# Performance work log

Measured on AMD Instinct MI355X. Metric: run time of the kernel, lower is better.

The kernel has to match this reference:

```python
import jax, jax.numpy as jnp
import numpy as np

NEG_SLOPE = 0.01  # torch F.leaky_relu default

def leaky_relu(x):
    return jnp.where(x >= 0, x, NEG_SLOPE * x)

def setup_inputs() -> dict:
    key = jax.random.key(0)
    ks = jax.random.split(key, 16)
    N, D, H, L = 2048, 512, 256, 16
    # normalized-adjacency-like matrix: row sums ~0.5 to keep activations sane
    A_hat = jax.random.uniform(ks[0], (N, N), dtype=jnp.float32) / N
    X = jax.random.normal(ks[1], (N, D), dtype=jnp.float32)
    eps = jax.random.normal(ks[2], (N, L), dtype=jnp.float32)
    def lin(k, fan_out, fan_in):
        s = 1.0 / np.sqrt(fan_in)
        kw, kb = jax.random.split(k)
        W = jax.random.uniform(kw, (fan_out, fan_in), minval=-s, maxval=s, dtype=jnp.float32)
        b = jax.random.uniform(kb, (fan_out,), minval=-s, maxval=s, dtype=jnp.float32)
        return W, b
    W1, b1 = lin(ks[3], H, D)          # gcn1
    Wmu, bmu = lin(ks[4], L, H)        # gcn2_mu
    Wlv, blv = lin(ks[5], L, H)        # gcn2_logvar
    Wd1, bd1 = lin(ks[6], 2 * L, 2 * L)  # decoder_fc1
    Wd2, bd2 = lin(ks[7], 1, 2 * L)      # decoder_fc2
    return {"A_hat": A_hat, "X": X, "eps": eps,
            "W1": W1, "b1": b1, "Wmu": Wmu, "bmu": bmu,
            "Wlv": Wlv, "blv": blv, "Wd1": Wd1, "bd1": bd1,
            "Wd2": Wd2, "bd2": bd2}

def reference(A_hat, X, eps, W1, b1, Wmu, bmu, Wlv, blv, Wd1, bd1, Wd2, bd2):
    L = Wmu.shape[0]
    # --- encode: two GCN layers (A_hat @ X) @ W.T + b ---
    Hh = leaky_relu((A_hat @ X) @ W1.T + b1)           # [N, H]
    AH = A_hat @ Hh                                    # [N, H]
    mu = AH @ Wmu.T + bmu                              # [N, L]
    logvar = AH @ Wlv.T + blv                          # [N, L]
    # --- reparameterize ---
    Z = mu + eps * jnp.exp(0.5 * logvar)               # [N, L]
    # --- decode: pairwise MLP on concat(Z_i, Z_j), vectorized ---
    # fc1(concat(Zi,Zj)) = Zi @ Wd1[:, :L].T + Zj @ Wd1[:, L:].T + bd1
    P = Z @ Wd1[:, :L].T                               # [N, 2L]
    Q = Z @ Wd1[:, L:].T                               # [N, 2L]
    h = leaky_relu(P[:, None, :] + Q[None, :, :] + bd1)  # [N, N, 2L]
    A_pred = jax.nn.sigmoid(jnp.einsum('nmh,h->nm', h, Wd2[0]) + bd2[0])  # [N, N]
    return (A_pred, mu, logvar)
```

## Files before the change

### kernel.cpp

```cpp
#include <hip/hip_runtime.h>

#define NNODE 2048
#define DD    512
#define HHID  256
#define LLAT  16
#define H2    32

typedef __attribute__((ext_vector_type(8))) short  short8;
typedef __attribute__((ext_vector_type(4))) float  f32x4;

__device__ __forceinline__ unsigned short f2bf(float x) {
    unsigned int u = __float_as_uint(x);
    unsigned int r = (u + 0x7fffu + ((u >> 16) & 1u)) >> 16;
    return (unsigned short)r;
}
__device__ __forceinline__ float bf2f(unsigned short u) {
    return __uint_as_float(((unsigned int)u) << 16);
}

__global__ __launch_bounds__(256) void t0_cvt(const float* __restrict__ A,
                                              const float* __restrict__ X,
                                              const float* __restrict__ W1,
                                              unsigned short* __restrict__ Abf,
                                              unsigned short* __restrict__ Xbf,
                                              unsigned short* __restrict__ W1bf) {
    const int NT = 1343488;
    for (int v = blockIdx.x * 256 + threadIdx.x; v < NT; v += gridDim.x * 256) {
        const float* src; unsigned short* dst; int off;
        if (v < 1048576)      { src = A;  dst = Abf;  off = v; }
        else if (v < 1310720) { src = X;  dst = Xbf;  off = v - 1048576; }
        else                  { src = W1; dst = W1bf; off = v - 1310720; }
        float4 f = ((const float4*)src)[off];
        short4 h;
        h.x = (short)f2bf(f.x); h.y = (short)f2bf(f.y);
        h.z = (short)f2bf(f.z); h.w = (short)f2bf(f.w);
        ((short4*)dst)[off] = h;
    }
}

__global__ __launch_bounds__(256) void t1_mfma(const unsigned short* __restrict__ W1bf,
                                               const unsigned short* __restrict__ Xbf,
                                               unsigned short* __restrict__ XWt) {
    const int wt   = blockIdx.x * 4 + (threadIdx.x >> 6);
    const int lane = threadIdx.x & 63;
    const int h0 = (wt >> 7) * 16;
    const int n0 = (wt & 127) * 16;
    const int lm = lane & 15, lk = (lane >> 4) * 8;
    const unsigned short* ap = W1bf + (size_t)(h0 + lm) * DD + lk;
    const unsigned short* bp = Xbf  + (size_t)(n0 + lm) * DD + lk;
    f32x4 acc = {};
    #pragma unroll 4
    for (int k = 0; k < DD; k += 32) {
        short8 a = *(const short8*)(ap + k);
        short8 b = *(const short8*)(bp + k);
        acc = __builtin_amdgcn_mfma_f32_16x16x32_bf16(a, b, acc, 0, 0, 0);
    }
    const int col = n0 + lm;
    #pragma unroll
    for (int r = 0; r < 4; ++r) {
        int row = h0 + (lane >> 4) * 4 + r;
        XWt[(size_t)row * NNODE + col] = f2bf(acc[r]);
    }
}

__global__ __launch_bounds__(256) void t2_mfma(const unsigned short* __restrict__ Abf,
                                               const unsigned short* __restrict__ XWt,
                                               const float* __restrict__ bias1,
                                               unsigned short* __restrict__ Hbf) {
    const int wt   = blockIdx.x * 4 + (threadIdx.x >> 6);
    const int lane = threadIdx.x & 63;
    const int m0 = (wt >> 3) * 16;
    const int n0 = (wt & 7) * 32;
    const int lm = lane & 15, lk = (lane >> 4) * 8;
    const unsigned short* ap  = Abf + (size_t)(m0 + lm) * NNODE + lk;
    const unsigned short* bp0 = XWt + (size_t)(n0 + lm) * NNODE + lk;
    const unsigned short* bp1 = XWt + (size_t)(n0 + 16 + lm) * NNODE + lk;
    f32x4 acc0 = {}, acc1 = {};
    #pragma unroll 4
    for (int k = 0; k < NNODE; k += 32) {
        short8 a  = *(const short8*)(ap + k);
        short8 b0 = *(const short8*)(bp0 + k);
        short8 b1 = *(const short8*)(bp1 + k);
        acc0 = __builtin_amdgcn_mfma_f32_16x16x32_bf16(a, b0, acc0, 0, 0, 0);
        acc1 = __builtin_amdgcn_mfma_f32_16x16x32_bf16(a, b1, acc1, 0, 0, 0);
    }
    const int col0 = n0 + lm, col1 = n0 + 16 + lm;
    const float bv0 = bias1[col0], bv1 = bias1[col1];
    #pragma unroll
    for (int r = 0; r < 4; ++r) {
        int row = m0 + (lane >> 4) * 4 + r;
        float v0 = acc0[r] + bv0;
        float v1 = acc1[r] + bv1;
        v0 = fmaxf(v0, 0.01f * v0);
        v1 = fmaxf(v1, 0.01f * v1);
        Hbf[(size_t)row * HHID + col0] = f2bf(v0);
        Hbf[(size_t)row * HHID + col1] = f2bf(v1);
    }
}

__global__ __launch_bounds__(256) void t3_g(const unsigned short* __restrict__ Hbf,
                                            const float* __restrict__ Wmu,
                                            const float* __restrict__ Wlv,
                                            unsigned short* __restrict__ Gt) {
    __shared__ float Hs[8][260];
    __shared__ float Ws[32][260];
    const int tid = threadIdx.x;
    const int n0 = blockIdx.x * 8;
    #pragma unroll
    for (int s = 0; s < 8; ++s) {
        int idx = tid + s * 256;
        int row = idx >> 6, c = (idx & 63) * 4;
        const float* src = (row < 16) ? (Wmu + (size_t)row * HHID)
                                      : (Wlv + (size_t)(row - 16) * HHID);
        *(float4*)&Ws[row][c] = *(const float4*)(src + c);
    }
    {
        int r = tid >> 5, seg = tid & 31;
        int d = seg * 8;
        ushort4 u0 = *(const ushort4*)(Hbf + (size_t)(n0 + r) * HHID + d);
        ushort4 u1 = *(const ushort4*)(Hbf + (size_t)(n0 + r) * HHID + d + 4);
        Hs[r][d + 0] = bf2f(u0.x); Hs[r][d + 1] = bf2f(u0.y);
        Hs[r][d + 2] = bf2f(u0.z); Hs[r][d + 3] = bf2f(u0.w);
        Hs[r][d + 4] = bf2f(u1.x); Hs[r][d + 5] = bf2f(u1.y);
        Hs[r][d + 6] = bf2f(u1.z); Hs[r][d + 7] = bf2f(u1.w);
    }
    __syncthreads();
    const int r = tid >> 5, j = tid & 31;
    float acc = 0.f;
    #pragma unroll 8
    for (int d4 = 0; d4 < 64; ++d4) {
        float4 a = *(const float4*)&Hs[r][d4 * 4];
        float4 b = *(const float4*)&Ws[j][d4 * 4];
        acc += a.x * b.x + a.y * b.y + a.z * b.z + a.w * b.w;
    }
    Gt[(size_t)j * NNODE + n0 + r] = f2bf(acc);
}

__global__ __launch_bounds__(256) void t4_mfma(const unsigned short* __restrict__ Abf,
                                               const unsigned short* __restrict__ Gt,
                                               float* __restrict__ Mp) {
    const int wt   = blockIdx.x * 4 + (threadIdx.x >> 6);
    const int lane = threadIdx.x & 63;
    const int m0 = (wt >> 4) * 16;
    const int nt = wt & 1;
    const int ks = (wt >> 1) & 7;
    const int n0 = nt * 16;
    const int kbase = ks * 256;
    const int lm = lane & 15, lk = (lane >> 4) * 8;
    const unsigned short* ap = Abf + (size_t)(m0 + lm) * NNODE + kbase + lk;
    const unsigned short* bp = Gt  + (size_t)(n0 + lm) * NNODE + kbase + lk;
    f32x4 acc = {};
    #pragma unroll
    for (int k = 0; k < 256; k += 32) {
        short8 a = *(const short8*)(ap + k);
        short8 b = *(const short8*)(bp + k);
        acc = __builtin_amdgcn_mfma_f32_16x16x32_bf16(a, b, acc, 0, 0, 0);
    }
    float* outp = Mp + (size_t)ks * 65536;
    const int col = n0 + lm;
    #pragma unroll
    for (int r = 0; r < 4; ++r) {
        int row = m0 + (lane >> 4) * 4 + r;
        outp[(size_t)row * H2 + col] = acc[r];
    }
}

__global__ __launch_bounds__(256) void t5_z(const float* __restrict__ Mp,
                                            const float* __restrict__ bmu,
                                            const float* __restrict__ blv,
                                            const float* __restrict__ eps,
                                            const float* __restrict__ Wd1,
                                            const float* __restrict__ bd1,
                                            float* __restrict__ out_mu,
                                            float* __restrict__ out_lv,
                                            float* __restrict__ Pp,
                                            float* __restrict__ Qq) {
    __shared__ float Zs[16][16];
    const int tid = threadIdx.x;
    const int n0 = blockIdx.x * 16;
    {
        int nl = tid >> 4, l = tid & 15;
        int n = n0 + nl;
        float m = bmu[l], lv = blv[l];
        #pragma unroll
        for (int s = 0; s < 8; ++s) {
            m  += Mp[(size_t)s * 65536 + (size_t)n * H2 + l];
            lv += Mp[(size_t)s * 65536 + (size_t)n * H2 + 16 + l];
        }
        out_mu[(size_t)n * LLAT + l] = m;
        out_lv[(size_t)n * LLAT + l] = lv;
        Zs[nl][l] = m + eps[(size_t)n * LLAT + l] * __expf(0.5f * lv);
    }
    __syncthreads();
    #pragma unroll
    for (int p = 0; p < 2; ++p) {
        int idx = tid + p * 256;
        int nl = idx >> 5, o = idx & 31;
        int n = n0 + nl;
        float ap = bd1[o], aq = 0.f;
        #pragma unroll
        for (int l = 0; l < 16; ++l) {
            float z = Zs[nl][l];
            ap = fmaf(z, Wd1[o * H2 + l],      ap);
            aq = fmaf(z, Wd1[o * H2 + 16 + l], aq);
        }
        Pp[(size_t)n * H2 + o] = ap;
        Qq[(size_t)n * H2 + o] = aq;
    }
}

__global__ __launch_bounds__(256) void t6_dec(const float* __restrict__ Pp,
                                              const float* __restrict__ Qq,
                                              const float* __restrict__ Wd2,
                                              const float* __restrict__ bd2,
                                              float* __restrict__ Apred) {
    __shared__ float Qt[32][68];
    __shared__ float Ws2[32];
    const int tid = threadIdx.x;
    const int j0 = blockIdx.x * 64, i0 = blockIdx.y * 16;
    #pragma unroll
    for (int s = 0; s < 8; ++s) {
        int idx = tid + s * 256;
        int j = idx >> 5, o = idx & 31;
        Qt[o][j] = Qq[(size_t)(j0 + j) * H2 + o];
    }
    if (tid < 32) Ws2[tid] = Wd2[tid];
    const int i = i0 + (tid >> 4);
    const int jq = tid & 15;
    float p[32];
    const float4* P4 = (const float4*)(Pp + (size_t)i * H2);
    #pragma unroll
    for (int c = 0; c < 8; ++c) {
        float4 v = P4[c];
        p[c * 4] = v.x; p[c * 4 + 1] = v.y; p[c * 4 + 2] = v.z; p[c * 4 + 3] = v.w;
    }
    __syncthreads();
    f32x4 acc = {0.f, 0.f, 0.f, 0.f};
    #pragma unroll
    for (int o = 0; o < 32; ++o) {
        float4 q = *(const float4*)&Qt[o][jq * 4];
        float w = Ws2[o], po = p[o];
        float s0 = po + q.x, s1 = po + q.y, s2 = po + q.z, s3 = po + q.w;
        acc[0] = fmaf(w, fmaxf(s0, 0.01f * s0), acc[0]);
        acc[1] = fmaf(w, fmaxf(s1, 0.01f * s1), acc[1]);
        acc[2] = fmaf(w, fmaxf(s2, 0.01f * s2), acc[2]);
        acc[3] = fmaf(w, fmaxf(s3, 0.01f * s3), acc[3]);
    }
    float b = bd2[0];
    float4 r;
    r.x = 1.f / (1.f + __expf(-(acc[0] + b)));
    r.y = 1.f / (1.f + __expf(-(acc[1] + b)));
    r.z = 1.f / (1.f + __expf(-(acc[2] + b)));
    r.w = 1.f / (1.f + __expf(-(acc[3] + b)));
    *(float4*)(Apred + (size_t)i * NNODE + j0 + jq * 4) = r;
}

extern "C" void kernel_launch(void* const* d_in, const int* in_sizes, int n_in,
                              void* d_out, int out_size, void* d_ws, size_t ws_size,
                              hipStream_t stream) {
    const float* A   = (const float*)d_in[0];
    const float* X   = (const float*)d_in[1];
    const float* eps = (const float*)d_in[2];
    const float* W1  = (const float*)d_in[3];
    const float* b1  = (const float*)d_in[4];
    const float* Wmu = (const float*)d_in[5];
    const float* bmu = (const float*)d_in[6];
    const float* Wlv = (const float*)d_in[7];
    const float* blv = (const float*)d_in[8];
    const float* Wd1 = (const float*)d_in[9];
    const float* bd1 = (const float*)d_in[10];
    const float* Wd2 = (const float*)d_in[11];
    const float* bd2 = (const float*)d_in[12];
    float* out = (float*)d_out;
    char* ws = (char*)d_ws;

    unsigned short* Abf  = (unsigned short*)(ws);
    unsigned short* Xbf  = (unsigned short*)(ws + 8388608);
    unsigned short* W1bf = (unsigned short*)(ws + 10485760);
    unsigned short* XWt  = (unsigned short*)(ws + 10747904);
    unsigned short* Hbf  = (unsigned short*)(ws + 11796480);
    unsigned short* Gt   = (unsigned short*)(ws + 12845056);
    float*          Mp   = (float*)(ws + 12976128);
    float*          Pp   = (float*)(ws + 15073280);
    float*          Qq   = (float*)(ws + 15335424);

    float* out_mu = out + (size_t)NNODE * NNODE;
    float* out_lv = out_mu + NNODE * LLAT;

    t0_cvt <<<1024,          256, 0, stream>>>(A, X, W1, Abf, Xbf, W1bf);
    t1_mfma<<<512,           256, 0, stream>>>(W1bf, Xbf, XWt);
    t2_mfma<<<256,           256, 0, stream>>>(Abf, XWt, b1, Hbf);
    t3_g   <<<256,           256, 0, stream>>>(Hbf, Wmu, Wlv, Gt);
    t4_mfma<<<512,           256, 0, stream>>>(Abf, Gt, Mp);
    t5_z   <<<128,           256, 0, stream>>>(Mp, bmu, blv, eps, Wd1, bd1,
                                               out_mu, out_lv, Pp, Qq);
    t6_dec <<<dim3(32, 128), 256, 0, stream>>>(Pp, Qq, Wd2, bd2, out);
}
```

Baseline: 160.2 us.

## Fuse all stages into one cooperative persistent kernel with grid syncs

Replaces the seven separate kernel launches with a single cooperative kernel of 256 blocks × 512 threads that runs every stage in sequence, separated by grid.sync(). The aim is to remove per-launch overhead and the gaps between launches. In exchange, each grid barrier adds its own cost and parallelism is capped at 256 blocks. Some stages also change their work split: t2 now gives each wave a single 16-wide tile, t3 splits each dot product across two lanes, and the decoder loops over 8 row groups per block.

```diff
diff --git a/kernel.cpp b/kernel.cpp
--- a/kernel.cpp
+++ b/kernel.cpp
@@ -1,4 +1,7 @@
 #include <hip/hip_runtime.h>
+#include <hip/hip_cooperative_groups.h>
+
+namespace cg = cooperative_groups;
 
 #define NNODE 2048
 #define DD    512
@@ -18,241 +21,221 @@
     return __uint_as_float(((unsigned int)u) << 16);
 }
 
-__global__ __launch_bounds__(256) void t0_cvt(const float* __restrict__ A,
-                                              const float* __restrict__ X,
-                                              const float* __restrict__ W1,
-                                              unsigned short* __restrict__ Abf,
-                                              unsigned short* __restrict__ Xbf,
-                                              unsigned short* __restrict__ W1bf) {
-    const int NT = 1343488;
-    for (int v = blockIdx.x * 256 + threadIdx.x; v < NT; v += gridDim.x * 256) {
-        const float* src; unsigned short* dst; int off;
-        if (v < 1048576)      { src = A;  dst = Abf;  off = v; }
-        else if (v < 1310720) { src = X;  dst = Xbf;  off = v - 1048576; }
-        else                  { src = W1; dst = W1bf; off = v - 1310720; }
-        float4 f = ((const float4*)src)[off];
-        short4 h;
-        h.x = (short)f2bf(f.x); h.y = (short)f2bf(f.y);
-        h.z = (short)f2bf(f.z); h.w = (short)f2bf(f.w);
-        ((short4*)dst)[off] = h;
-    }
-}
-
-__global__ __launch_bounds__(256) void t1_mfma(const unsigned short* __restrict__ W1bf,
-                                               const unsigned short* __restrict__ Xbf,
-                                               unsigned short* __restrict__ XWt) {
-    const int wt   = blockIdx.x * 4 + (threadIdx.x >> 6);
-    const int lane = threadIdx.x & 63;
-    const int h0 = (wt >> 7) * 16;
-    const int n0 = (wt & 127) * 16;
-    const int lm = lane & 15, lk = (lane >> 4) * 8;
-    const unsigned short* ap = W1bf + (size_t)(h0 + lm) * DD + lk;
-    const unsigned short* bp = Xbf  + (size_t)(n0 + lm) * DD + lk;
-    f32x4 acc = {};
-    #pragma unroll 4
-    for (int k = 0; k < DD; k += 32) {
-        short8 a = *(const short8*)(ap + k);
-        short8 b = *(const short8*)(bp + k);
-        acc = __builtin_amdgcn_mfma_f32_16x16x32_bf16(a, b, acc, 0, 0, 0);
-    }
-    const int col = n0 + lm;
-    #pragma unroll
-    for (int r = 0; r < 4; ++r) {
-        int row = h0 + (lane >> 4) * 4 + r;
-        XWt[(size_t)row * NNODE + col] = f2bf(acc[r]);
-    }
-}
-
-__global__ __launch_bounds__(256) void t2_mfma(const unsigned short* __restrict__ Abf,
-                                               const unsigned short* __restrict__ XWt,
-                                               const float* __restrict__ bias1,
-                                               unsigned short* __restrict__ Hbf) {
-    const int wt   = blockIdx.x * 4 + (threadIdx.x >> 6);
-    const int lane = threadIdx.x & 63;
-    const int m0 = (wt >> 3) * 16;
-    const int n0 = (wt & 7) * 32;
-    const int lm = lane & 15, lk = (lane >> 4) * 8;
-    const unsigned short* ap  = Abf + (size_t)(m0 + lm) * NNODE + lk;
-    const unsigned short* bp0 = XWt + (size_t)(n0 + lm) * NNODE + lk;
-    const unsigned short* bp1 = XWt + (size_t)(n0 + 16 + lm) * NNODE + lk;
-    f32x4 acc0 = {}, acc1 = {};
-    #pragma unroll 4
-    for (int k = 0; k < NNODE; k += 32) {
-        short8 a  = *(const short8*)(ap + k);
-        short8 b0 = *(const short8*)(bp0 + k);
-        short8 b1 = *(const short8*)(bp1 + k);
-        acc0 = __builtin_amdgcn_mfma_f32_16x16x32_bf16(a, b0, acc0, 0, 0, 0);
-        acc1 = __builtin_amdgcn_mfma_f32_16x16x32_bf16(a, b1, acc1, 0, 0, 0);
-    }
-    const int col0 = n0 + lm, col1 = n0 + 16 + lm;
-    const float bv0 = bias1[col0], bv1 = bias1[col1];
-    #pragma unroll
-    for (int r = 0; r < 4; ++r) {
-        int row = m0 + (lane >> 4) * 4 + r;
-        float v0 = acc0[r] + bv0;
-        float v1 = acc1[r] + bv1;
-        v0 = fmaxf(v0, 0.01f * v0);
-        v1 = fmaxf(v1, 0.01f * v1);
-        Hbf[(size_t)row * HHID + col0] = f2bf(v0);
-        Hbf[(size_t)row * HHID + col1] = f2bf(v1);
-    }
-}
-
-__global__ __launch_bounds__(256) void t3_g(const unsigned short* __restrict__ Hbf,
-                                            const float* __restrict__ Wmu,
-                                            const float* __restrict__ Wlv,
-                                            unsigned short* __restrict__ Gt) {
-    __shared__ float Hs[8][260];
-    __shared__ float Ws[32][260];
-    const int tid = threadIdx.x;
-    const int n0 = blockIdx.x * 8;
-    #pragma unroll
-    for (int s = 0; s < 8; ++s) {
-        int idx = tid + s * 256;
-        int row = idx >> 6, c = (idx & 63) * 4;
-        const float* src = (row < 16) ? (Wmu + (size_t)row * HHID)
-                                      : (Wlv + (size_t)(row - 16) * HHID);
-        *(float4*)&Ws[row][c] = *(const float4*)(src + c);
-    }
-    {
-        int r = tid >> 5, seg = tid & 31;
-        int d = seg * 8;
-        ushort4 u0 = *(const ushort4*)(Hbf + (size_t)(n0 + r) * HHID + d);
-        ushort4 u1 = *(const ushort4*)(Hbf + (size_t)(n0 + r) * HHID + d + 4);
-        Hs[r][d + 0] = bf2f(u0.x); Hs[r][d + 1] = bf2f(u0.y);
-        Hs[r][d + 2] = bf2f(u0.z); Hs[r][d + 3] = bf2f(u0.w);
-        Hs[r][d + 4] = bf2f(u1.x); Hs[r][d + 5] = bf2f(u1.y);
-        Hs[r][d + 6] = bf2f(u1.z); Hs[r][d + 7] = bf2f(u1.w);
-    }
-    __syncthreads();
-    const int r = tid >> 5, j = tid & 31;
-    float acc = 0.f;
-    #pragma unroll 8
-    for (int d4 = 0; d4 < 64; ++d4) {
-        float4 a = *(const float4*)&Hs[r][d4 * 4];
-        float4 b = *(const float4*)&Ws[j][d4 * 4];
-        acc += a.x * b.x + a.y * b.y + a.z * b.z + a.w * b.w;
-    }
-    Gt[(size_t)j * NNODE + n0 + r] = f2bf(acc);
-}
-
-__global__ __launch_bounds__(256) void t4_mfma(const unsigned short* __restrict__ Abf,
-                                               const unsigned short* __restrict__ Gt,
-                                               float* __restrict__ Mp) {
-    const int wt   = blockIdx.x * 4 + (threadIdx.x >> 6);
-    const int lane = threadIdx.x & 63;
-    const int m0 = (wt >> 4) * 16;
-    const int nt = wt & 1;
-    const int ks = (wt >> 1) & 7;
-    const int n0 = nt * 16;
-    const int kbase = ks * 256;
-    const int lm = lane & 15, lk = (lane >> 4) * 8;
-    const unsigned short* ap = Abf + (size_t)(m0 + lm) * NNODE + kbase + lk;
-    const unsigned short* bp = Gt  + (size_t)(n0 + lm) * NNODE + kbase + lk;
-    f32x4 acc = {};
-    #pragma unroll
-    for (int k = 0; k < 256; k += 32) {
-        short8 a = *(const short8*)(ap + k);
-        short8 b = *(const short8*)(bp + k);
-        acc = __builtin_amdgcn_mfma_f32_16x16x32_bf16(a, b, acc, 0, 0, 0);
-    }
-    float* outp = Mp + (size_t)ks * 65536;
-    const int col = n0 + lm;
-    #pragma unroll
-    for (int r = 0; r < 4; ++r) {
-        int row = m0 + (lane >> 4) * 4 + r;
-        outp[(size_t)row * H2 + col] = acc[r];
-    }
-}
-
-__global__ __launch_bounds__(256) void t5_z(const float* __restrict__ Mp,
-                                            const float* __restrict__ bmu,
-                                            const float* __restrict__ blv,
-                                            const float* __restrict__ eps,
-                                            const float* __restrict__ Wd1,
-                                            const float* __restrict__ bd1,
-                                            float* __restrict__ out_mu,
-                                            float* __restrict__ out_lv,
-                                            float* __restrict__ Pp,
-                                            float* __restrict__ Qq) {
-    __shared__ float Zs[16][16];
-    const int tid = threadIdx.x;
-    const int n0 = blockIdx.x * 16;
-    {
-        int nl = tid >> 4, l = tid & 15;
-        int n = n0 + nl;
-        float m = bmu[l], lv = blv[l];
-        #pragma unroll
-        for (int s = 0; s < 8; ++s) {
-            m  += Mp[(size_t)s * 65536 + (size_t)n * H2 + l];
-            lv += Mp[(size_t)s * 65536 + (size_t)n * H2 + 16 + l];
-        }
-        out_mu[(size_t)n * LLAT + l] = m;
-        out_lv[(size_t)n * LLAT + l] = lv;
-        Zs[nl][l] = m + eps[(size_t)n * LLAT + l] * __expf(0.5f * lv);
-    }
-    __syncthreads();
-    #pragma unroll
-    for (int p = 0; p < 2; ++p) {
-        int idx = tid + p * 256;
-        int nl = idx >> 5, o = idx & 31;
-        int n = n0 + nl;
-        float ap = bd1[o], aq = 0.f;
-        #pragma unroll
-        for (int l = 0; l < 16; ++l) {
-            float z = Zs[nl][l];
-            ap = fmaf(z, Wd1[o * H2 + l],      ap);
-            aq = fmaf(z, Wd1[o * H2 + 16 + l], aq);
-        }
-        Pp[(size_t)n * H2 + o] = ap;
-        Qq[(size_t)n * H2 + o] = aq;
-    }
-}
-
-__global__ __launch_bounds__(256) void t6_dec(const float* __restrict__ Pp,
-                                              const float* __restrict__ Qq,
-                                              const float* __restrict__ Wd2,
-                                              const float* __restrict__ bd2,
-                                              float* __restrict__ Apred) {
-    __shared__ float Qt[32][68];
-    __shared__ float Ws2[32];
-    const int tid = threadIdx.x;
-    const int j0 = blockIdx.x * 64, i0 = blockIdx.y * 16;
-    #pragma unroll
-    for (int s = 0; s < 8; ++s) {
-        int idx = tid + s * 256;
-        int j = idx >> 5, o = idx & 31;
-        Qt[o][j] = Qq[(size_t)(j0 + j) * H2 + o];
-    }
-    if (tid < 32) Ws2[tid] = Wd2[tid];
-    const int i = i0 + (tid >> 4);
-    const int jq = tid & 15;
-    float p[32];
-    const float4* P4 = (const float4*)(Pp + (size_t)i * H2);
-    #pragma unroll
-    for (int c = 0; c < 8; ++c) {
-        float4 v = P4[c];
-        p[c * 4] = v.x; p[c * 4 + 1] = v.y; p[c * 4 + 2] = v.z; p[c * 4 + 3] = v.w;
-    }
-    __syncthreads();
-    f32x4 acc = {0.f, 0.f, 0.f, 0.f};
-    #pragma unroll
-    for (int o = 0; o < 32; ++o) {
-        float4 q = *(const float4*)&Qt[o][jq * 4];
-        float w = Ws2[o], po = p[o];
-        float s0 = po + q.x, s1 = po + q.y, s2 = po + q.z, s3 = po + q.w;
-        acc[0] = fmaf(w, fmaxf(s0, 0.01f * s0), acc[0]);
-        acc[1] = fmaf(w, fmaxf(s1, 0.01f * s1), acc[1]);
-        acc[2] = fmaf(w, fmaxf(s2, 0.01f * s2), acc[2]);
-        acc[3] = fmaf(w, fmaxf(s3, 0.01f * s3), acc[3]);
-    }
-    float b = bd2[0];
-    float4 r;
-    r.x = 1.f / (1.f + __expf(-(acc[0] + b)));
-    r.y = 1.f / (1.f + __expf(-(acc[1] + b)));
-    r.z = 1.f / (1.f + __expf(-(acc[2] + b)));
-    r.w = 1.f / (1.f + __expf(-(acc[3] + b)));
-    *(float4*)(Apred + (size_t)i * NNODE + j0 + jq * 4) = r;
+__global__ __launch_bounds__(512) void vgae_mega(
+    const float* __restrict__ A,   const float* __restrict__ X,
+    const float* __restrict__ eps, const float* __restrict__ W1,
+    const float* __restrict__ b1,  const float* __restrict__ Wmu,
+    const float* __restrict__ bmu, const float* __restrict__ Wlv,
+    const float* __restrict__ blv, const float* __restrict__ Wd1,
+    const float* __restrict__ bd1, const float* __restrict__ Wd2,
+    const float* __restrict__ bd2,
+    float* __restrict__ Apred, float* __restrict__ out_mu, float* __restrict__ out_lv,
+    unsigned short* __restrict__ Abf, unsigned short* __restrict__ Xbf,
+    unsigned short* __restrict__ W1bf, unsigned short* __restrict__ XWt,
+    unsigned short* __restrict__ Hbf, unsigned short* __restrict__ Gt,
+    float* __restrict__ Mp, float* __restrict__ Pp, float* __restrict__ Qq)
+{
+    cg::grid_group grid = cg::this_grid();
+    __shared__ __align__(16) char smem[41728];
+
+    const int tid  = threadIdx.x;
+    const int bid  = blockIdx.x;
+    const int lane = tid & 63;
+    const int wib  = tid >> 6;
+    const int wid  = bid * 8 + wib;
+    const int lm   = lane & 15;
+    const int lkq  = lane >> 4;
+    const int lk   = lkq * 8;
+
+    {
+        const int NT4 = 1343488;
+        for (int v = bid * 512 + tid; v < NT4; v += 131072) {
+            const float* src; unsigned short* dst; int off;
+            if (v < 1048576)      { src = A;  dst = Abf;  off = v; }
+            else if (v < 1310720) { src = X;  dst = Xbf;  off = v - 1048576; }
+            else                  { src = W1; dst = W1bf; off = v - 1310720; }
+            float4 f = ((const float4*)src)[off];
+            short4 h;
+            h.x = (short)f2bf(f.x); h.y = (short)f2bf(f.y);
+            h.z = (short)f2bf(f.z); h.w = (short)f2bf(f.w);
+            ((short4*)dst)[off] = h;
+        }
+    }
+    grid.sync();
+
+    {
+        const int h0 = (wid >> 7) * 16;
+        const int n0 = (wid & 127) * 16;
+        const unsigned short* ap = W1bf + (size_t)(h0 + lm) * DD + lk;
+        const unsigned short* bp = Xbf  + (size_t)(n0 + lm) * DD + lk;
+        f32x4 acc = {};
+        #pragma unroll 4
+        for (int k = 0; k < DD; k += 32) {
+            short8 a = *(const short8*)(ap + k);
+            short8 b = *(const short8*)(bp + k);
+            acc = __builtin_amdgcn_mfma_f32_16x16x32_bf16(a, b, acc, 0, 0, 0);
+        }
+        #pragma unroll
+        for (int r = 0; r < 4; ++r)
+            XWt[(size_t)(h0 + lkq * 4 + r) * NNODE + n0 + lm] = f2bf(acc[r]);
+    }
+    grid.sync();
+
+    {
+        const int m0 = (wid >> 4) * 16;
+        const int n0 = (wid & 15) * 16;
+        const unsigned short* ap = Abf + (size_t)(m0 + lm) * NNODE + lk;
+        const unsigned short* bp = XWt + (size_t)(n0 + lm) * NNODE + lk;
+        f32x4 acc = {};
+        #pragma unroll 4
+        for (int k = 0; k < NNODE; k += 32) {
+            short8 a = *(const short8*)(ap + k);
+            short8 b = *(const short8*)(bp + k);
+            acc = __builtin_amdgcn_mfma_f32_16x16x32_bf16(a, b, acc, 0, 0, 0);
+        }
+        const int col = n0 + lm;
+        const float bv = b1[col];
+        #pragma unroll
+        for (int r = 0; r < 4; ++r) {
+            float v = acc[r] + bv;
+            v = fmaxf(v, 0.01f * v);
+            Hbf[(size_t)(m0 + lkq * 4 + r) * HHID + col] = f2bf(v);
+        }
+    }
+    grid.sync();
+
+    {
+        float (*Ws)[260] = (float(*)[260])smem;
+        float (*Hs)[260] = (float(*)[260])(smem + 33280);
+        const int n0 = bid * 8;
+        #pragma unroll
+        for (int s = 0; s < 4; ++s) {
+            int idx = tid + s * 512;
+            int row = idx >> 6, c = (idx & 63) * 4;
+            const float* src = (row < 16) ? (Wmu + (size_t)row * HHID)
+                                          : (Wlv + (size_t)(row - 16) * HHID);
+            *(float4*)&Ws[row][c] = *(const float4*)(src + c);
+        }
+        {
+            int r = tid >> 6, d = (tid & 63) * 4;
+            ushort4 u = *(const ushort4*)(Hbf + (size_t)(n0 + r) * HHID + d);
+            Hs[r][d + 0] = bf2f(u.x); Hs[r][d + 1] = bf2f(u.y);
+            Hs[r][d + 2] = bf2f(u.z); Hs[r][d + 3] = bf2f(u.w);
+        }
+        __syncthreads();
+        const int pair = tid >> 1, half = tid & 1;
+        const int r = pair >> 5, j = pair & 31;
+        float acc = 0.f;
+        #pragma unroll 8
+        for (int d4 = half * 32; d4 < half * 32 + 32; ++d4) {
+            float4 a = *(const float4*)&Hs[r][d4 * 4];
+            float4 b = *(const float4*)&Ws[j][d4 * 4];
+            acc += a.x * b.x + a.y * b.y + a.z * b.z + a.w * b.w;
+        }
+        float other = __shfl_xor(acc, 1);
+        if (half == 0) Gt[(size_t)j * NNODE + n0 + r] = f2bf(acc + other);
+    }
+    grid.sync();
+
+    {
+        const int m0 = (wid >> 4) * 16;
+        const int nt = wid & 1;
+        const int ks = (wid >> 1) & 7;
+        const int n0 = nt * 16;
+        const unsigned short* ap = Abf + (size_t)(m0 + lm) * NNODE + ks * 256 + lk;
+        const unsigned short* bp = Gt  + (size_t)(n0 + lm) * NNODE + ks * 256 + lk;
+        f32x4 acc = {};
+        #pragma unroll
+        for (int k = 0; k < 256; k += 32) {
+            short8 a = *(const short8*)(ap + k);
+            short8 b = *(const short8*)(bp + k);
+            acc = __builtin_amdgcn_mfma_f32_16x16x32_bf16(a, b, acc, 0, 0, 0);
+        }
+        float* outp = Mp + (size_t)ks * 65536;
+        const int col = n0 + lm;
+        #pragma unroll
+        for (int r = 0; r < 4; ++r)
+            outp[(size_t)(m0 + lkq * 4 + r) * H2 + col] = acc[r];
+    }
+    grid.sync();
+
+    {
+        float (*Zs)[16] = (float(*)[16])smem;
+        const int n0 = bid * 8;
+        if (tid < 128) {
+            int nl = tid >> 4, l = tid & 15;
+            int n = n0 + nl;
+            float m = bmu[l], lv = blv[l];
+            #pragma unroll
+            for (int s = 0; s < 8; ++s) {
+                m  += Mp[(size_t)s * 65536 + (size_t)n * H2 + l];
+                lv += Mp[(size_t)s * 65536 + (size_t)n * H2 + 16 + l];
+            }
+            out_mu[(size_t)n * LLAT + l] = m;
+            out_lv[(size_t)n * LLAT + l] = lv;
+            Zs[nl][l] = m + eps[(size_t)n * LLAT + l] * __expf(0.5f * lv);
+        }
+        __syncthreads();
+        if (tid < 256) {
+            int nl = tid >> 5, o = tid & 31;
+            int n = n0 + nl;
+            float ap_ = bd1[o], aq = 0.f;
+            #pragma unroll
+            for (int l = 0; l < 16; ++l) {
+                float z = Zs[nl][l];
+                ap_ = fmaf(z, Wd1[o * H2 + l],      ap_);
+                aq  = fmaf(z, Wd1[o * H2 + 16 + l], aq);
+            }
+            Pp[(size_t)n * H2 + o] = ap_;
+            Qq[(size_t)n * H2 + o] = aq;
+        }
+    }
+    grid.sync();
+
+    {
+        float (*Qt)[68] = (float(*)[68])smem;
+        float* Ws2 = (float*)(smem + 32 * 68 * 4);
+        const int j0    = (bid & 31) * 64;
+        const int ibase = (bid >> 5) * 256;
+        #pragma unroll
+        for (int s = 0; s < 4; ++s) {
+            int idx = tid + s * 512;
+            int j = idx >> 5, o = idx & 31;
+            Qt[o][j] = Qq[(size_t)(j0 + j) * H2 + o];
+        }
+        if (tid < 32) Ws2[tid] = Wd2[tid];
+        __syncthreads();
+        const float b2 = bd2[0];
+        const int jq = tid & 15;
+        #pragma unroll 2
+        for (int sub = 0; sub < 8; ++sub) {
+            const int i = ibase + sub * 32 + (tid >> 4);
+            float p[32];
+            const float4* P4 = (const float4*)(Pp + (size_t)i * H2);
+            #pragma unroll
+            for (int c = 0; c < 8; ++c) {
+                float4 v = P4[c];
+                p[c * 4] = v.x; p[c * 4 + 1] = v.y; p[c * 4 + 2] = v.z; p[c * 4 + 3] = v.w;
+            }
+            f32x4 acc = {0.f, 0.f, 0.f, 0.f};
+            #pragma unroll
+            for (int o = 0; o < 32; ++o) {
+                float4 q = *(const float4*)&Qt[o][jq * 4];
+                float w = Ws2[o], po = p[o];
+                float s0 = po + q.x, s1 = po + q.y, s2 = po + q.z, s3 = po + q.w;
+                acc[0] = fmaf(w, fmaxf(s0, 0.01f * s0), acc[0]);
+                acc[1] = fmaf(w, fmaxf(s1, 0.01f * s1), acc[1]);
+                acc[2] = fmaf(w, fmaxf(s2, 0.01f * s2), acc[2]);
+                acc[3] = fmaf(w, fmaxf(s3, 0.01f * s3), acc[3]);
+            }
+            float4 r;
+            r.x = 1.f / (1.f + __expf(-(acc[0] + b2)));
+            r.y = 1.f / (1.f + __expf(-(acc[1] + b2)));
+            r.z = 1.f / (1.f + __expf(-(acc[2] + b2)));
+            r.w = 1.f / (1.f + __expf(-(acc[3] + b2)));
+            *(float4*)(Apred + (size_t)i * NNODE + j0 + jq * 4) = r;
+        }
+    }
 }
 
 extern "C" void kernel_launch(void* const* d_in, const int* in_sizes, int n_in,
@@ -287,12 +270,14 @@
     float* out_mu = out + (size_t)NNODE * NNODE;
     float* out_lv = out_mu + NNODE * LLAT;
 
-    t0_cvt <<<1024,          256, 0, stream>>>(A, X, W1, Abf, Xbf, W1bf);
-    t1_mfma<<<512,           256, 0, stream>>>(W1bf, Xbf, XWt);
-    t2_mfma<<<256,           256, 0, stream>>>(Abf, XWt, b1, Hbf);
-    t3_g   <<<256,           256, 0, stream>>>(Hbf, Wmu, Wlv, Gt);
-    t4_mfma<<<512,           256, 0, stream>>>(Abf, Gt, Mp);
-    t5_z   <<<128,           256, 0, stream>>>(Mp, bmu, blv, eps, Wd1, bd1,
-                                               out_mu, out_lv, Pp, Qq);
-    t6_dec <<<dim3(32, 128), 256, 0, stream>>>(Pp, Qq, Wd2, bd2, out);
-}
+    void* args[] = {
+        (void*)&A, (void*)&X, (void*)&eps, (void*)&W1, (void*)&b1,
+        (void*)&Wmu, (void*)&bmu, (void*)&Wlv, (void*)&blv,
+        (void*)&Wd1, (void*)&bd1, (void*)&Wd2, (void*)&bd2,
+        (void*)&out, (void*)&out_mu, (void*)&out_lv,
+        (void*)&Abf, (void*)&Xbf, (void*)&W1bf, (void*)&XWt,
+        (void*)&Hbf, (void*)&Gt, (void*)&Mp, (void*)&Pp, (void*)&Qq
+    };
+    hipLaunchCooperativeKernel((void*)vgae_mega, dim3(256), dim3(512),
+                               args, 0, stream);
+}
```

Measured after the change: 353.2 us. 120% more time.

## Fuse conversion into XW GEMM and fuse reparameterization into decoder

Applied to the files above, without the earlier changes.

Folds the fp32-to-bf16 conversion of X and W1 into the first MFMA GEMM, which now reads fp32 and converts in registers, and also converts A in the same kernel. The Z/P/Q computation is merged into the pairwise decoder, so each block recomputes Z and P for 256 rows and Q for its 64 columns in shared memory. The second GEMM is retiled to one 16x16 output per wave. Together these cut kernel launches and intermediate global traffic, at the cost of redundant Z recomputation across blocks and fewer decoder blocks (256 blocks of 512 threads) with heavy shared memory use.

```diff
diff --git a/kernel.cpp b/kernel.cpp
--- a/kernel.cpp
+++ b/kernel.cpp
@@ -17,88 +17,78 @@
 __device__ __forceinline__ float bf2f(unsigned short u) {
     return __uint_as_float(((unsigned int)u) << 16);
 }
-
-__global__ __launch_bounds__(256) void t0_cvt(const float* __restrict__ A,
-                                              const float* __restrict__ X,
-                                              const float* __restrict__ W1,
-                                              unsigned short* __restrict__ Abf,
-                                              unsigned short* __restrict__ Xbf,
-                                              unsigned short* __restrict__ W1bf) {
-    const int NT = 1343488;
-    for (int v = blockIdx.x * 256 + threadIdx.x; v < NT; v += gridDim.x * 256) {
-        const float* src; unsigned short* dst; int off;
-        if (v < 1048576)      { src = A;  dst = Abf;  off = v; }
-        else if (v < 1310720) { src = X;  dst = Xbf;  off = v - 1048576; }
-        else                  { src = W1; dst = W1bf; off = v - 1310720; }
-        float4 f = ((const float4*)src)[off];
+__device__ __forceinline__ short8 cvt8(const float* p) {
+    float4 f0 = *(const float4*)p;
+    float4 f1 = *(const float4*)(p + 4);
+    short8 s;
+    s[0] = (short)f2bf(f0.x); s[1] = (short)f2bf(f0.y);
+    s[2] = (short)f2bf(f0.z); s[3] = (short)f2bf(f0.w);
+    s[4] = (short)f2bf(f1.x); s[5] = (short)f2bf(f1.y);
+    s[6] = (short)f2bf(f1.z); s[7] = (short)f2bf(f1.w);
+    return s;
+}
+
+__global__ __launch_bounds__(256) void k1_xw(const float* __restrict__ A,
+                                             const float* __restrict__ X,
+                                             const float* __restrict__ W1,
+                                             unsigned short* __restrict__ Abf,
+                                             unsigned short* __restrict__ XWt) {
+    const int tid = threadIdx.x, bid = blockIdx.x;
+    for (int v = bid * 256 + tid; v < 1048576; v += 131072) {
+        float4 f = ((const float4*)A)[v];
         short4 h;
         h.x = (short)f2bf(f.x); h.y = (short)f2bf(f.y);
         h.z = (short)f2bf(f.z); h.w = (short)f2bf(f.w);
-        ((short4*)dst)[off] = h;
-    }
-}
-
-__global__ __launch_bounds__(256) void t1_mfma(const unsigned short* __restrict__ W1bf,
-                                               const unsigned short* __restrict__ Xbf,
-                                               unsigned short* __restrict__ XWt) {
-    const int wt   = blockIdx.x * 4 + (threadIdx.x >> 6);
-    const int lane = threadIdx.x & 63;
-    const int h0 = (wt >> 7) * 16;
-    const int n0 = (wt & 127) * 16;
-    const int lm = lane & 15, lk = (lane >> 4) * 8;
-    const unsigned short* ap = W1bf + (size_t)(h0 + lm) * DD + lk;
-    const unsigned short* bp = Xbf  + (size_t)(n0 + lm) * DD + lk;
+        ((short4*)Abf)[v] = h;
+    }
+    const int wid  = bid * 4 + (tid >> 6);
+    const int lane = tid & 63;
+    const int h0 = (wid >> 7) * 16;
+    const int n0 = (wid & 127) * 16;
+    const int lm = lane & 15, lkq = lane >> 4, lk = lkq * 8;
+    const float* wp = W1 + (size_t)(h0 + lm) * DD + lk;
+    const float* xp = X  + (size_t)(n0 + lm) * DD + lk;
     f32x4 acc = {};
     #pragma unroll 4
     for (int k = 0; k < DD; k += 32) {
+        short8 a = cvt8(wp + k);
+        short8 b = cvt8(xp + k);
+        acc = __builtin_amdgcn_mfma_f32_16x16x32_bf16(a, b, acc, 0, 0, 0);
+    }
+    #pragma unroll
+    for (int r = 0; r < 4; ++r)
+        XWt[(size_t)(h0 + lkq * 4 + r) * NNODE + n0 + lm] = f2bf(acc[r]);
+}
+
+__global__ __launch_bounds__(256) void k2_h(const unsigned short* __restrict__ Abf,
+                                            const unsigned short* __restrict__ XWt,
+                                            const float* __restrict__ b1,
+                                            unsigned short* __restrict__ Hbf) {
+    const int wid  = blockIdx.x * 4 + (threadIdx.x >> 6);
+    const int lane = threadIdx.x & 63;
+    const int m0 = (wid >> 4) * 16;
+    const int n0 = (wid & 15) * 16;
+    const int lm = lane & 15, lkq = lane >> 4, lk = lkq * 8;
+    const unsigned short* ap = Abf + (size_t)(m0 + lm) * NNODE + lk;
+    const unsigned short* bp = XWt + (size_t)(n0 + lm) * NNODE + lk;
+    f32x4 acc = {};
+    #pragma unroll 4
+    for (int k = 0; k < NNODE; k += 32) {
         short8 a = *(const short8*)(ap + k);
         short8 b = *(const short8*)(bp + k);
         acc = __builtin_amdgcn_mfma_f32_16x16x32_bf16(a, b, acc, 0, 0, 0);
     }
     const int col = n0 + lm;
+    const float bv = b1[col];
     #pragma unroll
     for (int r = 0; r < 4; ++r) {
-        int row = h0 + (lane >> 4) * 4 + r;
-        XWt[(size_t)row * NNODE + col] = f2bf(acc[r]);
-    }
-}
-
-__global__ __launch_bounds__(256) void t2_mfma(const unsigned short* __restrict__ Abf,
-                                               const unsigned short* __restrict__ XWt,
-                                               const float* __restrict__ bias1,
-                                               unsigned short* __restrict__ Hbf) {
-    const int wt   = blockIdx.x * 4 + (threadIdx.x >> 6);
-    const int lane = threadIdx.x & 63;
-    const int m0 = (wt >> 3) * 16;
-    const int n0 = (wt & 7) * 32;
-    const int lm = lane & 15, lk = (lane >> 4) * 8;
-    const unsigned short* ap  = Abf + (size_t)(m0 + lm) * NNODE + lk;
-    const unsigned short* bp0 = XWt + (size_t)(n0 + lm) * NNODE + lk;
-    const unsigned short* bp1 = XWt + (size_t)(n0 + 16 + lm) * NNODE + lk;
-    f32x4 acc0 = {}, acc1 = {};
-    #pragma unroll 4
-    for (int k = 0; k < NNODE; k += 32) {
-        short8 a  = *(const short8*)(ap + k);
-        short8 b0 = *(const short8*)(bp0 + k);
-        short8 b1 = *(const short8*)(bp1 + k);
-        acc0 = __builtin_amdgcn_mfma_f32_16x16x32_bf16(a, b0, acc0, 0, 0, 0);
-        acc1 = __builtin_amdgcn_mfma_f32_16x16x32_bf16(a, b1, acc1, 0, 0, 0);
-    }
-    const int col0 = n0 + lm, col1 = n0 + 16 + lm;
-    const float bv0 = bias1[col0], bv1 = bias1[col1];
-    #pragma unroll
-    for (int r = 0; r < 4; ++r) {
-        int row = m0 + (lane >> 4) * 4 + r;
-        float v0 = acc0[r] + bv0;
-        float v1 = acc1[r] + bv1;
-        v0 = fmaxf(v0, 0.01f * v0);
-        v1 = fmaxf(v1, 0.01f * v1);
-        Hbf[(size_t)row * HHID + col0] = f2bf(v0);
-        Hbf[(size_t)row * HHID + col1] = f2bf(v1);
-    }
-}
-
-__global__ __launch_bounds__(256) void t3_g(const unsigned short* __restrict__ Hbf,
+        float v = acc[r] + bv;
+        v = fmaxf(v, 0.01f * v);
+        Hbf[(size_t)(m0 + lkq * 4 + r) * HHID + col] = f2bf(v);
+    }
+}
+
+__global__ __launch_bounds__(256) void k3_g(const unsigned short* __restrict__ Hbf,
                                             const float* __restrict__ Wmu,
                                             const float* __restrict__ Wlv,
                                             unsigned short* __restrict__ Gt) {
@@ -136,19 +126,18 @@
     Gt[(size_t)j * NNODE + n0 + r] = f2bf(acc);
 }
 
-__global__ __launch_bounds__(256) void t4_mfma(const unsigned short* __restrict__ Abf,
-                                               const unsigned short* __restrict__ Gt,
-                                               float* __restrict__ Mp) {
-    const int wt   = blockIdx.x * 4 + (threadIdx.x >> 6);
+__global__ __launch_bounds__(256) void k4_m(const unsigned short* __restrict__ Abf,
+                                            const unsigned short* __restrict__ Gt,
+                                            float* __restrict__ Mp) {
+    const int wid  = blockIdx.x * 4 + (threadIdx.x >> 6);
     const int lane = threadIdx.x & 63;
-    const int m0 = (wt >> 4) * 16;
-    const int nt = wt & 1;
-    const int ks = (wt >> 1) & 7;
+    const int m0 = (wid >> 4) * 16;
+    const int nt = wid & 1;
+    const int ks = (wid >> 1) & 7;
     const int n0 = nt * 16;
-    const int kbase = ks * 256;
-    const int lm = lane & 15, lk = (lane >> 4) * 8;
-    const unsigned short* ap = Abf + (size_t)(m0 + lm) * NNODE + kbase + lk;
-    const unsigned short* bp = Gt  + (size_t)(n0 + lm) * NNODE + kbase + lk;
+    const int lm = lane & 15, lkq = lane >> 4, lk = lkq * 8;
+    const unsigned short* ap = Abf + (size_t)(m0 + lm) * NNODE + ks * 256 + lk;
+    const unsigned short* bp = Gt  + (size_t)(n0 + lm) * NNODE + ks * 256 + lk;
     f32x4 acc = {};
     #pragma unroll
     for (int k = 0; k < 256; k += 32) {
@@ -159,100 +148,112 @@
     float* outp = Mp + (size_t)ks * 65536;
     const int col = n0 + lm;
     #pragma unroll
-    for (int r = 0; r < 4; ++r) {
-        int row = m0 + (lane >> 4) * 4 + r;
-        outp[(size_t)row * H2 + col] = acc[r];
-    }
-}
-
-__global__ __launch_bounds__(256) void t5_z(const float* __restrict__ Mp,
-                                            const float* __restrict__ bmu,
-                                            const float* __restrict__ blv,
-                                            const float* __restrict__ eps,
-                                            const float* __restrict__ Wd1,
-                                            const float* __restrict__ bd1,
-                                            float* __restrict__ out_mu,
-                                            float* __restrict__ out_lv,
-                                            float* __restrict__ Pp,
-                                            float* __restrict__ Qq) {
-    __shared__ float Zs[16][16];
+    for (int r = 0; r < 4; ++r)
+        outp[(size_t)(m0 + lkq * 4 + r) * H2 + col] = acc[r];
+}
+
+__global__ __launch_bounds__(512) void k5_dec(const float* __restrict__ Mp,
+                                              const float* __restrict__ bmu,
+                                              const float* __restrict__ blv,
+                                              const float* __restrict__ eps,
+                                              const float* __restrict__ Wd1,
+                                              const float* __restrict__ bd1,
+                                              const float* __restrict__ Wd2,
+                                              const float* __restrict__ bd2,
+                                              float* __restrict__ Apred,
+                                              float* __restrict__ out_mu,
+                                              float* __restrict__ out_lv) {
+    __shared__ float Zs[256][16];
+    __shared__ float Zjs[64][16];
+    __shared__ float Ps[256][32];
+    __shared__ float Qt[32][68];
+    __shared__ float Ws2[32];
     const int tid = threadIdx.x;
-    const int n0 = blockIdx.x * 16;
-    {
-        int nl = tid >> 4, l = tid & 15;
-        int n = n0 + nl;
+    const int jx = blockIdx.x;
+    const int j0 = jx * 64;
+    const int ibase = blockIdx.y * 256;
+    #pragma unroll
+    for (int p = 0; p < 8; ++p) {
+        int idx = tid + p * 512;
+        int nl = idx >> 4, l = idx & 15;
+        int n = ibase + nl;
         float m = bmu[l], lv = blv[l];
         #pragma unroll
         for (int s = 0; s < 8; ++s) {
             m  += Mp[(size_t)s * 65536 + (size_t)n * H2 + l];
             lv += Mp[(size_t)s * 65536 + (size_t)n * H2 + 16 + l];
         }
-        out_mu[(size_t)n * LLAT + l] = m;
-        out_lv[(size_t)n * LLAT + l] = lv;
+        if (jx == 0) {
+            out_mu[(size_t)n * LLAT + l] = m;
+            out_lv[(size_t)n * LLAT + l] = lv;
+        }
         Zs[nl][l] = m + eps[(size_t)n * LLAT + l] * __expf(0.5f * lv);
     }
+    #pragma unroll
+    for (int p = 0; p < 2; ++p) {
+        int idx = tid + p * 512;
+        int jl = idx >> 4, l = idx & 15;
+        int n = j0 + jl;
+        float m = bmu[l], lv = blv[l];
+        #pragma unroll
+        for (int s = 0; s < 8; ++s) {
+            m  += Mp[(size_t)s * 65536 + (size_t)n * H2 + l];
+            lv += Mp[(size_t)s * 65536 + (size_t)n * H2 + 16 + l];
+        }
+        Zjs[jl][l] = m + eps[(size_t)n * LLAT + l] * __expf(0.5f * lv);
+    }
+    if (tid < 32) Ws2[tid] = Wd2[tid];
     __syncthreads();
     #pragma unroll
-    for (int p = 0; p < 2; ++p) {
-        int idx = tid + p * 256;
+    for (int p = 0; p < 4; ++p) {
+        int idx = tid + p * 512;
+        int jl = idx >> 5, o = idx & 31;
+        float aq = 0.f;
+        #pragma unroll
+        for (int l = 0; l < 16; ++l)
+            aq = fmaf(Zjs[jl][l], Wd1[o * H2 + 16 + l], aq);
+        Qt[o][jl] = aq;
+    }
+    #pragma unroll
+    for (int p = 0; p < 16; ++p) {
+        int idx = tid + p * 512;
         int nl = idx >> 5, o = idx & 31;
-        int n = n0 + nl;
-        float ap = bd1[o], aq = 0.f;
-        #pragma unroll
-        for (int l = 0; l < 16; ++l) {
-            float z = Zs[nl][l];
-            ap = fmaf(z, Wd1[o * H2 + l],      ap);
-            aq = fmaf(z, Wd1[o * H2 + 16 + l], aq);
-        }
-        Pp[(size_t)n * H2 + o] = ap;
-        Qq[(size_t)n * H2 + o] = aq;
-    }
-}
-
-__global__ __launch_bounds__(256) void t6_dec(const float* __restrict__ Pp,
-                                              const float* __restrict__ Qq,
-                                              const float* __restrict__ Wd2,
-                                              const float* __restrict__ bd2,
-                                              float* __restrict__ Apred) {
-    __shared__ float Qt[32][68];
-    __shared__ float Ws2[32];
-    const int tid = threadIdx.x;
-    const int j0 = blockIdx.x * 64, i0 = blockIdx.y * 16;
-    #pragma unroll
-    for (int s = 0; s < 8; ++s) {
-        int idx = tid + s * 256;
-        int j = idx >> 5, o = idx & 31;
-        Qt[o][j] = Qq[(size_t)(j0 + j) * H2 + o];
-    }
-    if (tid < 32) Ws2[tid] = Wd2[tid];
-    const int i = i0 + (tid >> 4);
+        float ap = bd1[o];
+        #pragma unroll
+        for (int l = 0; l < 16; ++l)
+            ap = fmaf(Zs[nl][l], Wd1[o * H2 + l], ap);
+        Ps[nl][o] = ap;
+    }
+    __syncthreads();
+    const float b2 = bd2[0];
     const int jq = tid & 15;
-    float p[32];
-    const float4* P4 = (const float4*)(Pp + (size_t)i * H2);
-    #pragma unroll
-    for (int c = 0; c < 8; ++c) {
-        float4 v = P4[c];
-        p[c * 4] = v.x; p[c * 4 + 1] = v.y; p[c * 4 + 2] = v.z; p[c * 4 + 3] = v.w;
-    }
-    __syncthreads();
-    f32x4 acc = {0.f, 0.f, 0.f, 0.f};
-    #pragma unroll
-    for (int o = 0; o < 32; ++o) {
-        float4 q = *(const float4*)&Qt[o][jq * 4];
-        float w = Ws2[o], po = p[o];
-        float s0 = po + q.x, s1 = po + q.y, s2 = po + q.z, s3 = po + q.w;
-        acc[0] = fmaf(w, fmaxf(s0, 0.01f * s0), acc[0]);
-        acc[1] = fmaf(w, fmaxf(s1, 0.01f * s1), acc[1]);
-        acc[2] = fmaf(w, fmaxf(s2, 0.01f * s2), acc[2]);
-        acc[3] = fmaf(w, fmaxf(s3, 0.01f * s3), acc[3]);
-    }
-    float b = bd2[0];
-    float4 r;
-    r.x = 1.f / (1.f + __expf(-(acc[0] + b)));
-    r.y = 1.f / (1.f + __expf(-(acc[1] + b)));
-    r.z = 1.f / (1.f + __expf(-(acc[2] + b)));
-    r.w = 1.f / (1.f + __expf(-(acc[3] + b)));
-    *(float4*)(Apred + (size_t)i * NNODE + j0 + jq * 4) = r;
+    #pragma unroll 2
+    for (int sub = 0; sub < 8; ++sub) {
+        const int il = sub * 32 + (tid >> 4);
+        float p[32];
+        #pragma unroll
+        for (int c = 0; c < 8; ++c) {
+            float4 v = *(const float4*)&Ps[il][c * 4];
+            p[c * 4] = v.x; p[c * 4 + 1] = v.y; p[c * 4 + 2] = v.z; p[c * 4 + 3] = v.w;
+        }
+        f32x4 acc = {0.f, 0.f, 0.f, 0.f};
+        #pragma unroll
+        for (int o = 0; o < 32; ++o) {
+            float4 q = *(const float4*)&Qt[o][jq * 4];
+            float w = Ws2[o], po = p[o];
+            float s0 = po + q.x, s1 = po + q.y, s2 = po + q.z, s3 = po + q.w;
+            acc[0] = fmaf(w, fmaxf(s0, 0.01f * s0), acc[0]);
+            acc[1] = fmaf(w, fmaxf(s1, 0.01f * s1), acc[1]);
+            acc[2] = fmaf(w, fmaxf(s2, 0.01f * s2), acc[2]);
+            acc[3] = fmaf(w, fmaxf(s3, 0.01f * s3), acc[3]);
+        }
+        float4 r;
+        r.x = 1.f / (1.f + __expf(-(acc[0] + b2)));
+        r.y = 1.f / (1.f + __expf(-(acc[1] + b2)));
+        r.z = 1.f / (1.f + __expf(-(acc[2] + b2)));
+        r.w = 1.f / (1.f + __expf(-(acc[3] + b2)));
+        *(float4*)(Apred + (size_t)(ibase + il) * NNODE + j0 + jq * 4) = r;
+    }
 }
 
 extern "C" void kernel_launch(void* const* d_in, const int* in_sizes, int n_in,
@@ -274,25 +275,19 @@
     float* out = (float*)d_out;
     char* ws = (char*)d_ws;
 
-    unsigned short* Abf  = (unsigned short*)(ws);
-    unsigned short* Xbf  = (unsigned short*)(ws + 8388608);
-    unsigned short* W1bf = (unsigned short*)(ws + 10485760);
-    unsigned short* XWt  = (unsigned short*)(ws + 10747904);
-    unsigned short* Hbf  = (unsigned short*)(ws + 11796480);
-    unsigned short* Gt   = (unsigned short*)(ws + 12845056);
-    float*          Mp   = (float*)(ws + 12976128);
-    float*          Pp   = (float*)(ws + 15073280);
-    float*          Qq   = (float*)(ws + 15335424);
+    unsigned short* Abf = (unsigned short*)(ws);
+    unsigned short* XWt = (unsigned short*)(ws + 8388608);
+    unsigned short* Hbf = (unsigned short*)(ws + 9437184);
+    unsigned short* Gt  = (unsigned short*)(ws + 10485760);
+    float*          Mp  = (float*)(ws + 10616832);
 
     float* out_mu = out + (size_t)NNODE * NNODE;
     float* out_lv = out_mu + NNODE * LLAT;
 
-    t0_cvt <<<1024,          256, 0, stream>>>(A, X, W1, Abf, Xbf, W1bf);
-    t1_mfma<<<512,           256, 0, stream>>>(W1bf, Xbf, XWt);
-    t2_mfma<<<256,           256, 0, stream>>>(Abf, XWt, b1, Hbf);
-    t3_g   <<<256,           256, 0, stream>>>(Hbf, Wmu, Wlv, Gt);
-    t4_mfma<<<512,           256, 0, stream>>>(Abf, Gt, Mp);
-    t5_z   <<<128,           256, 0, stream>>>(Mp, bmu, blv, eps, Wd1, bd1,
-                                               out_mu, out_lv, Pp, Qq);
-    t6_dec <<<dim3(32, 128), 256, 0, stream>>>(Pp, Qq, Wd2, bd2, out);
-}
+    k1_xw <<<512,         256, 0, stream>>>(A, X, W1, Abf, XWt);
+    k2_h  <<<512,         256, 0, stream>>>(Abf, XWt, b1, Hbf);
+    k3_g  <<<256,         256, 0, stream>>>(Hbf, Wmu, Wlv, Gt);
+    k4_m  <<<512,         256, 0, stream>>>(Abf, Gt, Mp);
+    k5_dec<<<dim3(32, 8), 512, 0, stream>>>(Mp, bmu, blv, eps, Wd1, bd1, Wd2, bd2,
+                                            out, out_mu, out_lv);
+}
```

After: 192.2 us. +20.0%, slower.
